# Performance work log

Hardware: AMD Instinct MI355X
Metric: run time of the kernel (lower is better)

## Reference

```python
import jax, jax.numpy as jnp
import numpy as np
import math

D_MODEL = 1024
NUM_HEADS = 16
MAX_LEN = 2048
D_HEAD = D_MODEL // NUM_HEADS
BATCH = 2
SEQ = 2048


def setup_inputs() -> dict:
    root = jax.random.key(0)
    ks = jax.random.split(root, 10)
    s = 1.0 / math.sqrt(D_MODEL)
    return {
        "query": jax.random.normal(ks[0], (BATCH, SEQ, D_MODEL), jnp.float32),
        "key": jax.random.normal(ks[1], (BATCH, SEQ, D_MODEL), jnp.float32),
        "value": jax.random.normal(ks[2], (BATCH, SEQ, D_MODEL), jnp.float32),
        "Wq": jax.random.normal(ks[3], (D_MODEL, D_MODEL), jnp.float32) * s,
        "bq": jax.random.normal(ks[4], (D_MODEL,), jnp.float32) * s,
        "Wk": jax.random.normal(ks[5], (D_MODEL, D_MODEL), jnp.float32) * s,
        "bk": jax.random.normal(ks[6], (D_MODEL,), jnp.float32) * s,
        "Wv": jax.random.normal(ks[7], (D_MODEL, D_MODEL), jnp.float32) * s,
        "bv": jax.random.normal(ks[8], (D_MODEL,), jnp.float32) * s,
        "Er": jax.random.normal(ks[9], (MAX_LEN, D_HEAD), jnp.float32),
    }


def _skew(QEr):
    # QEr: [B, H, S, S] -> pad one zero column on the left, reshape, drop first row
    B, H, R, C = QEr.shape
    padded = jnp.pad(QEr, ((0, 0), (0, 0), (0, 0), (1, 0)))  # [B,H,R,C+1]
    reshaped = padded.reshape(B, H, C + 1, R)
    return reshaped[:, :, 1:, :]  # [B,H,R,C] == Srel


def reference(query, key, value, Wq, bq, Wk, bk, Wv, bv, Er):
    B, S, D = query.shape
    H, dh = NUM_HEADS, D_HEAD
    # nn.Linear: x @ W.T + b
    q = (jnp.einsum("bsd,ed->bse", query, Wq) + bq).reshape(B, S, H, dh).transpose(0, 2, 1, 3)  # [B,H,S,dh]
    k = (jnp.einsum("bsd,ed->bse", key, Wk) + bk).reshape(B, S, H, dh).transpose(0, 2, 1, 3)
    v = (jnp.einsum("bsd,ed->bse", value, Wv) + bv).reshape(B, S, H, dh).transpose(0, 2, 1, 3)
    start = MAX_LEN - S
    Er_s = Er[start:, :]  # [S, dh]
    QEr = jnp.einsum("bhsd,ld->bhsl", q, Er_s)  # [B,H,S,S]
    Srel = _skew(QEr)
    QK = jnp.einsum("bhsd,bhtd->bhst", q, k)
    attn = (QK + Srel) / math.sqrt(dh)
    causal = jnp.tril(jnp.ones((S, S), dtype=bool))
    attn = jnp.where(causal[None, None], attn, -jnp.inf)
    attn = jax.nn.softmax(attn, axis=-1)
    out = jnp.einsum("bhst,bhtd->bhsd", attn, v)  # [B,H,S,dh]
    out = out.transpose(0, 2, 1, 3).reshape(B, S, D)
    return out  # dropout is identity in eval mode
```

## Files before the change

kernel.cpp:

```cpp
#include <hip/hip_runtime.h>
#include <hip/hip_bf16.h>

typedef __attribute__((ext_vector_type(8))) short bf16x8;
typedef __attribute__((ext_vector_type(4))) float f32x4;

#define DEVI __device__ __forceinline__
#define AS1 __attribute__((address_space(1)))
#define AS3 __attribute__((address_space(3)))

constexpr int SEQ_   = 2048;
constexpr int HEADS  = 16;
constexpr int DHEAD  = 64;
constexpr int DMODEL = 1024;

DEVI unsigned short f2bf(float x) {
  __hip_bfloat16 h = __float2bfloat16(x);
  return __builtin_bit_cast(unsigned short, h);
}

DEVI f32x4 MFMA(bf16x8 a, bf16x8 b, f32x4 c) {
  return __builtin_amdgcn_mfma_f32_16x16x32_bf16(a, b, c, 0, 0, 0);
}

DEVI unsigned int cvtpk(float lo, float hi) {
  unsigned int u;
  asm("v_cvt_pk_bf16_f32 %0, %1, %2" : "=v"(u) : "v"(lo), "v"(hi));
  return u;
}

__global__ void conv3_kernel(const float* s0, const float* s1, const float* s2,
                             unsigned short* d0, unsigned short* d1, unsigned short* d2,
                             int n) {
  const float* s = (blockIdx.y == 0) ? s0 : (blockIdx.y == 1) ? s1 : s2;
  unsigned short* d = (blockIdx.y == 0) ? d0 : (blockIdx.y == 1) ? d1 : d2;
  int i = (blockIdx.x * 256 + threadIdx.x) * 8;
  if (i >= n) return;
  const float4* p = (const float4*)(s + i);
  float4 v0 = p[0], v1 = p[1];
  union { unsigned short u[8]; bf16x8 v; } t;
  t.u[0] = f2bf(v0.x); t.u[1] = f2bf(v0.y); t.u[2] = f2bf(v0.z); t.u[3] = f2bf(v0.w);
  t.u[4] = f2bf(v1.x); t.u[5] = f2bf(v1.y); t.u[6] = f2bf(v1.z); t.u[7] = f2bf(v1.w);
  *(bf16x8*)(d + i) = t.v;
}

__global__ void conv4_kernel(const float* s0, const float* s1, const float* s2,
                             const float* s3,
                             unsigned short* d0, unsigned short* d1,
                             unsigned short* d2, unsigned short* d3,
                             int n_w, int n_e) {
  const int y = blockIdx.y;
  const float* s = (y == 0) ? s0 : (y == 1) ? s1 : (y == 2) ? s2 : s3;
  unsigned short* d = (y == 0) ? d0 : (y == 1) ? d1 : (y == 2) ? d2 : d3;
  const int n = (y == 3) ? n_e : n_w;
  int i = (blockIdx.x * 256 + threadIdx.x) * 8;
  if (i >= n) return;
  const float4* p = (const float4*)(s + i);
  float4 v0 = p[0], v1 = p[1];
  union { unsigned short u[8]; bf16x8 v; } t;
  t.u[0] = f2bf(v0.x); t.u[1] = f2bf(v0.y); t.u[2] = f2bf(v0.z); t.u[3] = f2bf(v0.w);
  t.u[4] = f2bf(v1.x); t.u[5] = f2bf(v1.y); t.u[6] = f2bf(v1.z); t.u[7] = f2bf(v1.w);
  *(bf16x8*)(d + i) = t.v;
}

__global__ __launch_bounds__(256) void proj3_kernel(
    const unsigned short* __restrict__ X0, const unsigned short* __restrict__ X1,
    const unsigned short* __restrict__ X2,
    const unsigned short* __restrict__ W0, const unsigned short* __restrict__ W1,
    const unsigned short* __restrict__ W2,
    const float* __restrict__ bi0, const float* __restrict__ bi1,
    const float* __restrict__ bi2,
    unsigned short* __restrict__ o0, unsigned short* __restrict__ o1,
    unsigned short* __restrict__ o2) {
  const int z = blockIdx.z;
  const unsigned short* X = (z == 0) ? X0 : (z == 1) ? X1 : X2;
  const unsigned short* W = (z == 0) ? W0 : (z == 1) ? W1 : W2;
  const float* bias        = (z == 0) ? bi0 : (z == 1) ? bi1 : bi2;
  unsigned short* out      = (z == 0) ? o0 : (z == 1) ? o1 : o2;

  __shared__ unsigned short Abuf[2][128 * 32];
  __shared__ unsigned short Bbuf[2][128 * 32];
  const int tid  = threadIdx.x;
  const int lane = tid & 63, wv = tid >> 6;
  const int q = lane >> 4, r = lane & 15;
  const int wrow = wv >> 1, wcol = wv & 1;
  const int rowA0 = blockIdx.x * 128, colB0 = blockIdx.y * 128;

  const char* Ag = (const char*)(X + (size_t)rowA0 * DMODEL);
  const char* Bg = (const char*)(W + (size_t)colB0 * DMODEL);

  f32x4 acc[4][4] = {};

  auto stage = [&](int ks, int buf) {
    const int koff = ks * 64;
#pragma unroll
    for (int i = 0; i < 2; ++i) {
      const int b   = (i * 256 + tid) * 16;
      const int row = b >> 6, col = b & 63;
      __builtin_amdgcn_global_load_lds(
          (const AS1 void*)(Ag + (size_t)row * (DMODEL * 2) + koff + col),
          (AS3 void*)((char*)&Abuf[buf][0] + i * 4096 + wv * 1024),
          16, 0, 0);
      __builtin_amdgcn_global_load_lds(
          (const AS1 void*)(Bg + (size_t)row * (DMODEL * 2) + koff + col),
          (AS3 void*)((char*)&Bbuf[buf][0] + i * 4096 + wv * 1024),
          16, 0, 0);
    }
  };

  stage(0, 0);
  for (int ks = 0; ks < 32; ++ks) {
    __syncthreads();
    if (ks + 1 < 32) stage(ks + 1, (ks + 1) & 1);
    const unsigned short* A  = &Abuf[ks & 1][0];
    const unsigned short* Bt = &Bbuf[ks & 1][0];
    bf16x8 af[4], bfr[4];
#pragma unroll
    for (int t = 0; t < 4; ++t) {
      af[t]  = *(const bf16x8*)(A  + (wrow * 64 + t * 16 + r) * 32 + q * 8);
      bfr[t] = *(const bf16x8*)(Bt + (wcol * 64 + t * 16 + r) * 32 + q * 8);
    }
#pragma unroll
    for (int m = 0; m < 4; ++m)
#pragma unroll
      for (int n = 0; n < 4; ++n)
        acc[m][n] = MFMA(af[m], bfr[n], acc[m][n]);
  }

#pragma unroll
  for (int m = 0; m < 4; ++m) {
#pragma unroll
    for (int n = 0; n < 4; ++n) {
      const int e  = colB0 + wcol * 64 + n * 16 + r;
      const float bv = bias[e];
      const int h = e >> 6, dd = e & 63;
      const int nrow0 = rowA0 + wrow * 64 + m * 16 + q * 4;
      const int bb = nrow0 >> 11, ss0 = nrow0 & 2047;
      const size_t bh = (size_t)(bb * HEADS + h);
      if (z == 0) {
#pragma unroll
        for (int j = 0; j < 4; ++j)
          out[(bh * SEQ_ + (ss0 + j)) * DHEAD + dd] = f2bf((acc[m][n][j] + bv) * 0.125f);
      } else if (z == 1) {
#pragma unroll
        for (int j = 0; j < 4; ++j) {
          const int s = ss0 + j;
          const size_t off = (bh * 64 + (size_t)(s >> 5)) * 2048
                           + (size_t)(((dd >> 5) * 2 + ((s >> 4) & 1)) * 512)
                           + (size_t)(((((dd & 31) >> 3) << 4) + (s & 15)) * 8)
                           + (dd & 7);
          out[off] = f2bf(acc[m][n][j] + bv);
        }
      } else {
#pragma unroll
        for (int j = 0; j < 4; ++j) {
          const int s = ss0 + j;
          const int tile64 = s >> 6, t = s & 63;
          const int tp = 4 * (t & 15) + (t >> 4);
          const int tc = tp >> 5, u = tp & 31;
          const int ln = ((u >> 3) << 4) | (dd & 15);
          const size_t off = (bh * 32 + (size_t)tile64) * 4096
                           + (size_t)(tc * 2048 + (dd >> 4) * 512 + ln * 8 + (u & 7));
          out[off] = f2bf(acc[m][n][j] + bv);
        }
      }
    }
  }
}

struct ErSet { bf16x8 e[8]; };

__global__ __launch_bounds__(256, 2) void attn_kernel(
    const unsigned short* __restrict__ qb, const unsigned short* __restrict__ kt,
    const unsigned short* __restrict__ vt, const unsigned short* __restrict__ Er,
    float* __restrict__ out, float* __restrict__ pO1, float* __restrict__ pL) {
  __shared__ unsigned short k_lds[3][4096];
  __shared__ unsigned short v_lds[3][4096];
  __shared__ unsigned short p_lds[4][32][68];

  const int tid  = threadIdx.x;
  const int lane = tid & 63, wv = tid >> 6;
  const int q = lane >> 4, r = lane & 15;

  const int lid = blockIdx.x;
  const int xcd = lid & 7, idx = lid >> 3;
  const int bh  = (xcd << 2) | (idx & 3);
  const int jb  = idx >> 2;
  const int p = jb >> 1, role = jb & 1;
  const int bb = bh >> 4, hh = bh & 15;

  const unsigned short* qbh = qb + (size_t)bh * SEQ_ * DHEAD;
  const char* ktb = (const char*)(kt + (size_t)bh * 64 * 2048);
  const char* vtb = (const char*)(vt + (size_t)bh * 32 * 4096);
  const f32x4 zero4 = {0.f, 0.f, 0.f, 0.f};

  const char* sgbase = (wv < 2) ? ktb : vtb;
  char* sdst0 = (char*)((wv < 2) ? &k_lds[0][0] : &v_lds[0][0]);
  const int shalf = (wv & 1) * 4096;
  const int soff  = lane * 16;

  auto stageKV = [&](int it, int buf) {
    const char* src = sgbase + (size_t)it * 8192 + shalf + soff;
    char* dst = sdst0 + buf * 8192 + shalf;
#pragma unroll
    for (int c = 0; c < 4; ++c)
      __builtin_amdgcn_global_load_lds((const AS1 void*)(src + c * 1024),
                                       (AS3 void*)(dst + c * 1024), 16, 0, 0);
  };

  auto run_strip = [&](int T, int it0, int it1, float* po, float* pl) {
    const int s0 = T * 128 + wv * 32;
    __syncthreads();
    stageKV(it0, 0);

    bf16x8 qf[2][2];
#pragma unroll
    for (int rt = 0; rt < 2; ++rt) {
      qf[rt][0] = *(const bf16x8*)(qbh + (size_t)(s0 + rt * 16 + r) * DHEAD + q * 8);
      qf[rt][1] = *(const bf16x8*)(qbh + (size_t)(s0 + rt * 16 + r) * DHEAD + 32 + q * 8);
    }

    f32x4 qer[2][6];
    {
      const int lb0 = 2016 + it0 * 64 - s0;
#pragma unroll
      for (int m = 0; m < 2; ++m) {
        int l = lb0 + m * 16 + r; l = l < 2047 ? l : 2047;
        bf16x8 e0 = *(const bf16x8*)(Er + (size_t)l * DHEAD + q * 8);
        bf16x8 e1 = *(const bf16x8*)(Er + (size_t)l * DHEAD + 32 + q * 8);
#pragma unroll
        for (int rt = 0; rt < 2; ++rt)
          qer[rt][m] = MFMA(qf[rt][1], e1, MFMA(qf[rt][0], e0, zero4));
      }
    }

    auto loadE = [&](ErSet& es, int it) {
      const int lb = 2016 + it * 64 - s0;
#pragma unroll
      for (int mi = 0; mi < 4; ++mi) {
        int l = lb + 32 + mi * 16 + r;
        l = l < 2047 ? l : 2047;
        es.e[mi * 2 + 0] = *(const bf16x8*)(Er + (size_t)l * DHEAD + q * 8);
        es.e[mi * 2 + 1] = *(const bf16x8*)(Er + (size_t)l * DHEAD + 32 + q * 8);
      }
    };

    f32x4 oacc[2][4] = {};
    float lpart[2][4] = {};

    auto body = [&](int it, int cur, const ErSet& es) {
      const int t0 = it * 64;
      if (t0 > s0 + 31) return;
      const unsigned short* KL = &k_lds[cur][0];
      const unsigned short* VL = &v_lds[cur][0];

      bf16x8 kf[4][2];
#pragma unroll
      for (int ct = 0; ct < 4; ++ct)
#pragma unroll
        for (int kc = 0; kc < 2; ++kc)
          kf[ct][kc] = *(const bf16x8*)(KL + (ct >> 1) * 2048 + (kc * 2 + (ct & 1)) * 512 + lane * 8);

      f32x4 s4[2][4];
      __builtin_amdgcn_s_setprio(1);
#pragma unroll
      for (int rt = 0; rt < 2; ++rt)
#pragma unroll
        for (int ct = 0; ct < 4; ++ct)
          s4[rt][ct] = MFMA(qf[rt][1], kf[ct][1], MFMA(qf[rt][0], kf[ct][0], zero4));
#pragma unroll
      for (int rt = 0; rt < 2; ++rt)
#pragma unroll
        for (int mi = 0; mi < 4; ++mi)
          qer[rt][2 + mi] = MFMA(qf[rt][1], es.e[mi * 2 + 1],
                                 MFMA(qf[rt][0], es.e[mi * 2 + 0], zero4));
      __builtin_amdgcn_s_setprio(0);

      const int d0 = t0 - s0;
#pragma unroll
      for (int rt = 0; rt < 2; ++rt) {
        const int a = 1 - rt;
#pragma unroll
        for (int j = 0; j < 4; ++j) {
          unsigned int pkA = cvtpk(qer[rt][a][j],     qer[rt][a + 1][j]);
          unsigned int pkB = cvtpk(qer[rt][a + 2][j], qer[rt][a + 3][j]);
          const float  s5f = qer[rt][a + 4][j];
          const int srcl = (q << 4) | ((15 + r - q * 4 - j) & 15);
          unsigned int A = (unsigned int)__shfl((int)pkA, srcl);
          unsigned int B = (unsigned int)__shfl((int)pkB, srcl);
          const float g4 = __shfl(s5f, srcl);
          const float g0 = __builtin_bit_cast(float, A << 16);
          const float g1 = __builtin_bit_cast(float, A & 0xffff0000u);
          const float g2 = __builtin_bit_cast(float, B << 16);
          const float g3 = __builtin_bit_cast(float, B & 0xffff0000u);
          const bool hi = (r > q * 4 + j);
          const float b0 = hi ? g1 : g0;
          const float b1 = hi ? g2 : g1;
          const float b2 = hi ? g3 : g2;
          const float b3 = hi ? g4 : g3;
          const int A_ = rt * 16 + q * 4 + j - r - d0;
          const float p0 = (A_ >= 0)  ? __expf(s4[rt][0][j] + b0) : 0.f;
          const float p1 = (A_ >= 16) ? __expf(s4[rt][1][j] + b1) : 0.f;
          const float p2 = (A_ >= 32) ? __expf(s4[rt][2][j] + b2) : 0.f;
          const float p3 = (A_ >= 48) ? __expf(s4[rt][3][j] + b3) : 0.f;
          lpart[rt][j] += (p0 + p1) + (p2 + p3);
          const int sl = rt * 16 + q * 4 + j;
          const unsigned long long pw =
              (unsigned long long)cvtpk(p0, p1) |
              ((unsigned long long)cvtpk(p2, p3) << 32);
          *(unsigned long long*)&p_lds[wv][sl][4 * r] = pw;
        }
      }

      bf16x8 vf[4][2];
#pragma unroll
      for (int dc = 0; dc < 4; ++dc)
#pragma unroll
        for (int tc = 0; tc < 2; ++tc)
          vf[dc][tc] = *(const bf16x8*)(VL + tc * 2048 + dc * 512 + lane * 8);
      __builtin_amdgcn_s_setprio(1);
#pragma unroll
      for (int rt = 0; rt < 2; ++rt) {
        bf16x8 pf0 = *(const bf16x8*)(&p_lds[wv][rt * 16 + r][0] + q * 8);
        bf16x8 pf1 = *(const bf16x8*)(&p_lds[wv][rt * 16 + r][0] + 32 + q * 8);
#pragma unroll
        for (int dc = 0; dc < 4; ++dc)
          oacc[rt][dc] = MFMA(pf1, vf[dc][1], MFMA(pf0, vf[dc][0], oacc[rt][dc]));
      }
      __builtin_amdgcn_s_setprio(0);

#pragma unroll
      for (int rt = 0; rt < 2; ++rt) { qer[rt][0] = qer[rt][4]; qer[rt][1] = qer[rt][5]; }
    };

    ErSet eA, eB;
    loadE(eA, it0);

    int it = it0, cur = 0;
    while (true) {
      int nx = cur + 1; if (nx == 3) nx = 0;
      int itn = (it + 1 < it1) ? it + 1 : it1 - 1;
      stageKV(itn, nx);
      loadE(eB, itn);
      asm volatile("s_waitcnt vmcnt(12)\n\ts_barrier" ::: "memory");
      body(it, cur, eA);
      cur = nx;
      if (++it >= it1) break;
      nx = cur + 1; if (nx == 3) nx = 0;
      itn = (it + 1 < it1) ? it + 1 : it1 - 1;
      stageKV(itn, nx);
      loadE(eA, itn);
      asm volatile("s_waitcnt vmcnt(12)\n\ts_barrier" ::: "memory");
      body(it, cur, eB);
      cur = nx;
      if (++it >= it1) break;
    }

#pragma unroll
    for (int rt = 0; rt < 2; ++rt)
#pragma unroll
      for (int j = 0; j < 4; ++j) {
        float ls = lpart[rt][j];
#pragma unroll
        for (int d = 1; d < 16; d <<= 1) ls += __shfl_xor(ls, d);
        const int row = wv * 32 + rt * 16 + q * 4 + j;
        if (po) {
#pragma unroll
          for (int dc = 0; dc < 4; ++dc)
            po[(size_t)row * 64 + dc * 16 + r] = oacc[rt][dc][j];
        } else {
          const int ss = T * 128 + row;
#pragma unroll
          for (int dc = 0; dc < 4; ++dc)
            out[((size_t)(bb * SEQ_ + ss)) * DMODEL + hh * DHEAD + dc * 16 + r] = oacc[rt][dc][j];
        }
        if (r == 0) pl[row] = ls;
      }
  };

  int TA, a1, TB, b0, b1;
  if (role == 0) { TA = 15 - p; a1 = 16 - p; TB = p;      b0 = p + 1;  b1 = 2 * p + 2; }
  else           { TA = p;      a1 = p + 1;  TB = 15 - p; b0 = 16 - p; b1 = 32 - 2 * p; }

  run_strip(TA, 0, a1, nullptr,
            pL + ((size_t)(bh * 16 + TA)) * 256);
  run_strip(TB, b0, b1, pO1 + ((size_t)(bh * 16 + TB)) * 8192,
            pL + ((size_t)(bh * 16 + TB)) * 256 + 128);
}

__global__ __launch_bounds__(256) void reduce_kernel(const float* __restrict__ pO1,
                                                     const float* __restrict__ pL,
                                                     float* __restrict__ out) {
  const int slot = blockIdx.x;
  const int bh = slot >> 4, T = slot & 15;
  const int bb = bh >> 4, hh = bh & 15;
  const int tid = threadIdx.x;
  const int row = tid >> 1, half = (tid & 1) * 32;

  const float l0 = pL[(size_t)slot * 256 + row];
  const float l1 = pL[(size_t)slot * 256 + 128 + row];
  const float inv = 1.0f / (l0 + l1);

  float* a = out + ((size_t)(bb * SEQ_) + T * 128 + row) * DMODEL + hh * DHEAD + half;
  const float* b = pO1 + (size_t)slot * 8192 + row * 64 + half;
#pragma unroll
  for (int k = 0; k < 8; ++k) {
    float4 x = ((const float4*)a)[k];
    float4 y = ((const float4*)b)[k];
    float4 o;
    o.x = (x.x + y.x) * inv; o.y = (x.y + y.y) * inv;
    o.z = (x.z + y.z) * inv; o.w = (x.w + y.w) * inv;
    ((float4*)a)[k] = o;
  }
}

extern "C" void kernel_launch(void* const* d_in, const int* in_sizes, int n_in,
                              void* d_out, int out_size, void* d_ws, size_t ws_size,
                              hipStream_t stream) {
  const float* query = (const float*)d_in[0];
  const float* key   = (const float*)d_in[1];
  const float* value = (const float*)d_in[2];
  const float* Wq    = (const float*)d_in[3];
  const float* bq    = (const float*)d_in[4];
  const float* Wk    = (const float*)d_in[5];
  const float* bk    = (const float*)d_in[6];
  const float* Wv    = (const float*)d_in[7];
  const float* bv    = (const float*)d_in[8];
  const float* Er    = (const float*)d_in[9];

  char* ws = (char*)d_ws;
  unsigned short* qb   = (unsigned short*)(ws + (0u  << 20));
  unsigned short* ktil = (unsigned short*)(ws + (8u  << 20));
  unsigned short* vtil = (unsigned short*)(ws + (16u << 20));
  float*          pO1  = (float*)(ws + (24u << 20));
  float*          pL   = (float*)(ws + (40u << 20));
  unsigned short* Xq   = (unsigned short*)(ws + (32u << 20));
  unsigned short* Xk   = (unsigned short*)(ws + (40u << 20));
  unsigned short* Xv   = (unsigned short*)(ws + (48u << 20));
  unsigned short* Wqb  = (unsigned short*)(ws + (56u << 20));
  unsigned short* Wkb  = (unsigned short*)(ws + (58u << 20));
  unsigned short* Wvb  = (unsigned short*)(ws + (60u << 20));
  unsigned short* Erb  = (unsigned short*)(ws + (62u << 20));

  conv3_kernel<<<dim3(2048, 3), 256, 0, stream>>>(query, key, value, Xq, Xk, Xv,
                                                  2 * SEQ_ * DMODEL);
  conv4_kernel<<<dim3(512, 4), 256, 0, stream>>>(Wq, Wk, Wv, Er,
                                                 Wqb, Wkb, Wvb, Erb,
                                                 DMODEL * DMODEL, SEQ_ * DHEAD);

  proj3_kernel<<<dim3(32, 8, 3), 256, 0, stream>>>(Xq, Xk, Xv, Wqb, Wkb, Wvb,
                                                   bq, bk, bv, qb, ktil, vtil);

  attn_kernel<<<dim3(512), 256, 0, stream>>>(qb, ktil, vtil, Erb,
                                             (float*)d_out, pO1, pL);

  reduce_kernel<<<dim3(512), 256, 0, stream>>>(pO1, pL, (float*)d_out);
}
```

Measured before the change: 141.3 us.

## Split causal attention strips into four KV chunks with 32-wide tiles and bf16 partials

Every query strip now splits its causal KV range into four equal chunks, each handled by a separate block. The grid doubles to 1024 blocks, and the reduce kernel merges four partial outputs. Tiles shrink from 64 to 32 keys, the V layout from the projection changes to match, and LDS buffers are halved so the launch bound can allow four blocks per CU. Partial outputs are stored as bf16, and exp is replaced by exp2 with log2(e) folded into the Q scale. This is meant to balance causal work across blocks and raise occupancy, at the cost of more partial-output traffic, smaller MFMA batches per step, and bf16 rounding of the partials.

```diff
diff --git a/kernel.cpp b/kernel.cpp
--- a/kernel.cpp
+++ b/kernel.cpp
@@ -139,7 +139,8 @@
       if (z == 0) {
 #pragma unroll
         for (int j = 0; j < 4; ++j)
-          out[(bh * SEQ_ + (ss0 + j)) * DHEAD + dd] = f2bf((acc[m][n][j] + bv) * 0.125f);
+          out[(bh * SEQ_ + (ss0 + j)) * DHEAD + dd] =
+              f2bf((acc[m][n][j] + bv) * 0.1803368801111244f);
       } else if (z == 1) {
 #pragma unroll
         for (int j = 0; j < 4; ++j) {
@@ -154,12 +155,12 @@
 #pragma unroll
         for (int j = 0; j < 4; ++j) {
           const int s = ss0 + j;
-          const int tile64 = s >> 6, t = s & 63;
-          const int tp = 4 * (t & 15) + (t >> 4);
-          const int tc = tp >> 5, u = tp & 31;
-          const int ln = ((u >> 3) << 4) | (dd & 15);
-          const size_t off = (bh * 32 + (size_t)tile64) * 4096
-                           + (size_t)(tc * 2048 + (dd >> 4) * 512 + ln * 8 + (u & 7));
+          const int t = s & 31;
+          const int tp = 2 * (t & 15) + (t >> 4);
+          const size_t off = (bh * 64 + (size_t)(s >> 5)) * 2048
+                           + (size_t)((dd >> 4) * 512)
+                           + (size_t)(((((tp >> 3) << 4) | (dd & 15))) * 8)
+                           + (tp & 7);
           out[off] = f2bf(acc[m][n][j] + bv);
         }
       }
@@ -167,15 +168,15 @@
   }
 }
 
-struct ErSet { bf16x8 e[8]; };
-
-__global__ __launch_bounds__(256, 2) void attn_kernel(
+struct ErSet { bf16x8 e[4]; };
+
+__global__ __launch_bounds__(256, 4) void attn_kernel(
     const unsigned short* __restrict__ qb, const unsigned short* __restrict__ kt,
     const unsigned short* __restrict__ vt, const unsigned short* __restrict__ Er,
-    float* __restrict__ out, float* __restrict__ pO1, float* __restrict__ pL) {
-  __shared__ unsigned short k_lds[3][4096];
-  __shared__ unsigned short v_lds[3][4096];
-  __shared__ unsigned short p_lds[4][32][68];
+    unsigned short* __restrict__ pO, float* __restrict__ pL) {
+  __shared__ unsigned short k_lds[3][2048];
+  __shared__ unsigned short v_lds[3][2048];
+  __shared__ unsigned short p_lds[4][32][40];
 
   const int tid  = threadIdx.x;
   const int lane = tid & 63, wv = tid >> 6;
@@ -184,33 +185,32 @@
   const int lid = blockIdx.x;
   const int xcd = lid & 7, idx = lid >> 3;
   const int bh  = (xcd << 2) | (idx & 3);
-  const int jb  = idx >> 2;
-  const int p = jb >> 1, role = jb & 1;
-  const int bb = bh >> 4, hh = bh & 15;
+  const int rest = idx >> 2;
+  const int p = rest >> 2, qq = rest & 3;
 
   const unsigned short* qbh = qb + (size_t)bh * SEQ_ * DHEAD;
   const char* ktb = (const char*)(kt + (size_t)bh * 64 * 2048);
-  const char* vtb = (const char*)(vt + (size_t)bh * 32 * 4096);
+  const char* vtb = (const char*)(vt + (size_t)bh * 64 * 2048);
   const f32x4 zero4 = {0.f, 0.f, 0.f, 0.f};
 
   const char* sgbase = (wv < 2) ? ktb : vtb;
   char* sdst0 = (char*)((wv < 2) ? &k_lds[0][0] : &v_lds[0][0]);
-  const int shalf = (wv & 1) * 4096;
+  const int shalf = (wv & 1) * 2048;
   const int soff  = lane * 16;
 
-  auto stageKV = [&](int it, int buf) {
-    const char* src = sgbase + (size_t)it * 8192 + shalf + soff;
-    char* dst = sdst0 + buf * 8192 + shalf;
-#pragma unroll
-    for (int c = 0; c < 4; ++c)
-      __builtin_amdgcn_global_load_lds((const AS1 void*)(src + c * 1024),
-                                       (AS3 void*)(dst + c * 1024), 16, 0, 0);
+  auto stage = [&](int it, int buf) {
+    const char* src = sgbase + (size_t)it * 4096 + shalf + soff;
+    char* dst = sdst0 + buf * 4096 + shalf;
+    __builtin_amdgcn_global_load_lds((const AS1 void*)(src),
+                                     (AS3 void*)(dst), 16, 0, 0);
+    __builtin_amdgcn_global_load_lds((const AS1 void*)(src + 1024),
+                                     (AS3 void*)(dst + 1024), 16, 0, 0);
   };
 
-  auto run_strip = [&](int T, int it0, int it1, float* po, float* pl) {
+  auto run_strip = [&](int T, int it0, int it1, unsigned short* po, float* pl) {
     const int s0 = T * 128 + wv * 32;
     __syncthreads();
-    stageKV(it0, 0);
+    stage(it0, 0);
 
     bf16x8 qf[2][2];
 #pragma unroll
@@ -219,12 +219,12 @@
       qf[rt][1] = *(const bf16x8*)(qbh + (size_t)(s0 + rt * 16 + r) * DHEAD + 32 + q * 8);
     }
 
-    f32x4 qer[2][6];
+    f32x4 qer[2][4];
     {
-      const int lb0 = 2016 + it0 * 64 - s0;
+      const int B0 = 2016 + 32 * it0 - s0;
 #pragma unroll
       for (int m = 0; m < 2; ++m) {
-        int l = lb0 + m * 16 + r; l = l < 2047 ? l : 2047;
+        int l = B0 + m * 16 + r; l = l < 2047 ? l : 2047;
         bf16x8 e0 = *(const bf16x8*)(Er + (size_t)l * DHEAD + q * 8);
         bf16x8 e1 = *(const bf16x8*)(Er + (size_t)l * DHEAD + 32 + q * 8);
 #pragma unroll
@@ -234,10 +234,10 @@
     }
 
     auto loadE = [&](ErSet& es, int it) {
-      const int lb = 2016 + it * 64 - s0;
-#pragma unroll
-      for (int mi = 0; mi < 4; ++mi) {
-        int l = lb + 32 + mi * 16 + r;
+      const int B0 = 2016 + 32 * it - s0;
+#pragma unroll
+      for (int mi = 0; mi < 2; ++mi) {
+        int l = B0 + 32 + mi * 16 + r;
         l = l < 2047 ? l : 2047;
         es.e[mi * 2 + 0] = *(const bf16x8*)(Er + (size_t)l * DHEAD + q * 8);
         es.e[mi * 2 + 1] = *(const bf16x8*)(Er + (size_t)l * DHEAD + 32 + q * 8);
@@ -248,29 +248,29 @@
     float lpart[2][4] = {};
 
     auto body = [&](int it, int cur, const ErSet& es) {
-      const int t0 = it * 64;
+      const int t0 = it * 32;
       if (t0 > s0 + 31) return;
       const unsigned short* KL = &k_lds[cur][0];
       const unsigned short* VL = &v_lds[cur][0];
 
-      bf16x8 kf[4][2];
-#pragma unroll
-      for (int ct = 0; ct < 4; ++ct)
+      bf16x8 kf[2][2];
+#pragma unroll
+      for (int ct = 0; ct < 2; ++ct)
 #pragma unroll
         for (int kc = 0; kc < 2; ++kc)
-          kf[ct][kc] = *(const bf16x8*)(KL + (ct >> 1) * 2048 + (kc * 2 + (ct & 1)) * 512 + lane * 8);
-
-      f32x4 s4[2][4];
+          kf[ct][kc] = *(const bf16x8*)(KL + (kc * 2 + ct) * 512 + lane * 8);
+
+      f32x4 s4[2][2];
       __builtin_amdgcn_s_setprio(1);
 #pragma unroll
       for (int rt = 0; rt < 2; ++rt)
 #pragma unroll
-        for (int ct = 0; ct < 4; ++ct)
+        for (int ct = 0; ct < 2; ++ct)
           s4[rt][ct] = MFMA(qf[rt][1], kf[ct][1], MFMA(qf[rt][0], kf[ct][0], zero4));
 #pragma unroll
       for (int rt = 0; rt < 2; ++rt)
 #pragma unroll
-        for (int mi = 0; mi < 4; ++mi)
+        for (int mi = 0; mi < 2; ++mi)
           qer[rt][2 + mi] = MFMA(qf[rt][1], es.e[mi * 2 + 1],
                                  MFMA(qf[rt][0], es.e[mi * 2 + 0], zero4));
       __builtin_amdgcn_s_setprio(0);
@@ -281,55 +281,41 @@
         const int a = 1 - rt;
 #pragma unroll
         for (int j = 0; j < 4; ++j) {
-          unsigned int pkA = cvtpk(qer[rt][a][j],     qer[rt][a + 1][j]);
-          unsigned int pkB = cvtpk(qer[rt][a + 2][j], qer[rt][a + 3][j]);
-          const float  s5f = qer[rt][a + 4][j];
+          const unsigned int pk = cvtpk(qer[rt][a][j], qer[rt][a + 1][j]);
+          const float f2 = qer[rt][a + 2][j];
           const int srcl = (q << 4) | ((15 + r - q * 4 - j) & 15);
-          unsigned int A = (unsigned int)__shfl((int)pkA, srcl);
-          unsigned int B = (unsigned int)__shfl((int)pkB, srcl);
-          const float g4 = __shfl(s5f, srcl);
+          const unsigned int A = (unsigned int)__shfl((int)pk, srcl);
+          const float g2 = __shfl(f2, srcl);
           const float g0 = __builtin_bit_cast(float, A << 16);
           const float g1 = __builtin_bit_cast(float, A & 0xffff0000u);
-          const float g2 = __builtin_bit_cast(float, B << 16);
-          const float g3 = __builtin_bit_cast(float, B & 0xffff0000u);
           const bool hi = (r > q * 4 + j);
           const float b0 = hi ? g1 : g0;
           const float b1 = hi ? g2 : g1;
-          const float b2 = hi ? g3 : g2;
-          const float b3 = hi ? g4 : g3;
           const int A_ = rt * 16 + q * 4 + j - r - d0;
-          const float p0 = (A_ >= 0)  ? __expf(s4[rt][0][j] + b0) : 0.f;
-          const float p1 = (A_ >= 16) ? __expf(s4[rt][1][j] + b1) : 0.f;
-          const float p2 = (A_ >= 32) ? __expf(s4[rt][2][j] + b2) : 0.f;
-          const float p3 = (A_ >= 48) ? __expf(s4[rt][3][j] + b3) : 0.f;
-          lpart[rt][j] += (p0 + p1) + (p2 + p3);
+          const float p0 = (A_ >= 0)  ? exp2f(s4[rt][0][j] + b0) : 0.f;
+          const float p1 = (A_ >= 16) ? exp2f(s4[rt][1][j] + b1) : 0.f;
+          lpart[rt][j] += p0 + p1;
           const int sl = rt * 16 + q * 4 + j;
-          const unsigned long long pw =
-              (unsigned long long)cvtpk(p0, p1) |
-              ((unsigned long long)cvtpk(p2, p3) << 32);
-          *(unsigned long long*)&p_lds[wv][sl][4 * r] = pw;
+          *(unsigned int*)&p_lds[wv][sl][2 * r] = cvtpk(p0, p1);
         }
       }
 
-      bf16x8 vf[4][2];
+      bf16x8 vf[4];
 #pragma unroll
       for (int dc = 0; dc < 4; ++dc)
-#pragma unroll
-        for (int tc = 0; tc < 2; ++tc)
-          vf[dc][tc] = *(const bf16x8*)(VL + tc * 2048 + dc * 512 + lane * 8);
+        vf[dc] = *(const bf16x8*)(VL + dc * 512 + lane * 8);
       __builtin_amdgcn_s_setprio(1);
 #pragma unroll
       for (int rt = 0; rt < 2; ++rt) {
-        bf16x8 pf0 = *(const bf16x8*)(&p_lds[wv][rt * 16 + r][0] + q * 8);
-        bf16x8 pf1 = *(const bf16x8*)(&p_lds[wv][rt * 16 + r][0] + 32 + q * 8);
+        bf16x8 pf = *(const bf16x8*)(&p_lds[wv][rt * 16 + r][0] + q * 8);
 #pragma unroll
         for (int dc = 0; dc < 4; ++dc)
-          oacc[rt][dc] = MFMA(pf1, vf[dc][1], MFMA(pf0, vf[dc][0], oacc[rt][dc]));
+          oacc[rt][dc] = MFMA(pf, vf[dc], oacc[rt][dc]);
       }
       __builtin_amdgcn_s_setprio(0);
 
 #pragma unroll
-      for (int rt = 0; rt < 2; ++rt) { qer[rt][0] = qer[rt][4]; qer[rt][1] = qer[rt][5]; }
+      for (int rt = 0; rt < 2; ++rt) { qer[rt][0] = qer[rt][2]; qer[rt][1] = qer[rt][3]; }
     };
 
     ErSet eA, eB;
@@ -339,17 +325,17 @@
     while (true) {
       int nx = cur + 1; if (nx == 3) nx = 0;
       int itn = (it + 1 < it1) ? it + 1 : it1 - 1;
-      stageKV(itn, nx);
+      stage(itn, nx);
       loadE(eB, itn);
-      asm volatile("s_waitcnt vmcnt(12)\n\ts_barrier" ::: "memory");
+      asm volatile("s_waitcnt vmcnt(6)\n\ts_barrier" ::: "memory");
       body(it, cur, eA);
       cur = nx;
       if (++it >= it1) break;
       nx = cur + 1; if (nx == 3) nx = 0;
       itn = (it + 1 < it1) ? it + 1 : it1 - 1;
-      stageKV(itn, nx);
+      stage(itn, nx);
       loadE(eA, itn);
-      asm volatile("s_waitcnt vmcnt(12)\n\ts_barrier" ::: "memory");
+      asm volatile("s_waitcnt vmcnt(6)\n\ts_barrier" ::: "memory");
       body(it, cur, eB);
       cur = nx;
       if (++it >= it1) break;
@@ -363,31 +349,23 @@
 #pragma unroll
         for (int d = 1; d < 16; d <<= 1) ls += __shfl_xor(ls, d);
         const int row = wv * 32 + rt * 16 + q * 4 + j;
-        if (po) {
-#pragma unroll
-          for (int dc = 0; dc < 4; ++dc)
-            po[(size_t)row * 64 + dc * 16 + r] = oacc[rt][dc][j];
-        } else {
-          const int ss = T * 128 + row;
-#pragma unroll
-          for (int dc = 0; dc < 4; ++dc)
-            out[((size_t)(bb * SEQ_ + ss)) * DMODEL + hh * DHEAD + dc * 16 + r] = oacc[rt][dc][j];
-        }
+#pragma unroll
+        for (int dc = 0; dc < 4; ++dc)
+          po[(size_t)row * 64 + dc * 16 + r] = f2bf(oacc[rt][dc][j]);
         if (r == 0) pl[row] = ls;
       }
   };
 
-  int TA, a1, TB, b0, b1;
-  if (role == 0) { TA = 15 - p; a1 = 16 - p; TB = p;      b0 = p + 1;  b1 = 2 * p + 2; }
-  else           { TA = p;      a1 = p + 1;  TB = 15 - p; b0 = 16 - p; b1 = 32 - 2 * p; }
-
-  run_strip(TA, 0, a1, nullptr,
-            pL + ((size_t)(bh * 16 + TA)) * 256);
-  run_strip(TB, b0, b1, pO1 + ((size_t)(bh * 16 + TB)) * 8192,
-            pL + ((size_t)(bh * 16 + TB)) * 256 + 128);
-}
-
-__global__ __launch_bounds__(256) void reduce_kernel(const float* __restrict__ pO1,
+  const int TA = 15 - p, lenA = 16 - p;
+  const int TB = p,      lenB = p + 1;
+  const size_t slotA = ((size_t)bh * 16 + TA) * 4 + qq;
+  const size_t slotB = ((size_t)bh * 16 + TB) * 4 + qq;
+
+  run_strip(TA, qq * lenA, (qq + 1) * lenA, pO + slotA * 8192, pL + slotA * 128);
+  run_strip(TB, qq * lenB, (qq + 1) * lenB, pO + slotB * 8192, pL + slotB * 128);
+}
+
+__global__ __launch_bounds__(256) void reduce_kernel(const unsigned short* __restrict__ pO,
                                                      const float* __restrict__ pL,
                                                      float* __restrict__ out) {
   const int slot = blockIdx.x;
@@ -396,20 +374,32 @@
   const int tid = threadIdx.x;
   const int row = tid >> 1, half = (tid & 1) * 32;
 
-  const float l0 = pL[(size_t)slot * 256 + row];
-  const float l1 = pL[(size_t)slot * 256 + 128 + row];
-  const float inv = 1.0f / (l0 + l1);
-
-  float* a = out + ((size_t)(bb * SEQ_) + T * 128 + row) * DMODEL + hh * DHEAD + half;
-  const float* b = pO1 + (size_t)slot * 8192 + row * 64 + half;
-#pragma unroll
-  for (int k = 0; k < 8; ++k) {
-    float4 x = ((const float4*)a)[k];
-    float4 y = ((const float4*)b)[k];
+  float l = 0.f;
+#pragma unroll
+  for (int k = 0; k < 4; ++k) l += pL[((size_t)slot * 4 + k) * 128 + row];
+  const float inv = 1.0f / l;
+
+  float acc[32] = {};
+#pragma unroll
+  for (int k = 0; k < 4; ++k) {
+    const unsigned short* src = pO + ((size_t)slot * 4 + k) * 8192 + row * 64 + half;
+#pragma unroll
+    for (int c = 0; c < 4; ++c) {
+      union { bf16x8 v; unsigned short u[8]; } w;
+      w.v = *(const bf16x8*)(src + c * 8);
+#pragma unroll
+      for (int e = 0; e < 8; ++e)
+        acc[c * 8 + e] += __builtin_bit_cast(float, (unsigned int)w.u[e] << 16);
+    }
+  }
+
+  float* dst = out + ((size_t)(bb * SEQ_) + T * 128 + row) * DMODEL + hh * DHEAD + half;
+#pragma unroll
+  for (int c = 0; c < 8; ++c) {
     float4 o;
-    o.x = (x.x + y.x) * inv; o.y = (x.y + y.y) * inv;
-    o.z = (x.z + y.z) * inv; o.w = (x.w + y.w) * inv;
-    ((float4*)a)[k] = o;
+    o.x = acc[c * 4 + 0] * inv; o.y = acc[c * 4 + 1] * inv;
+    o.z = acc[c * 4 + 2] * inv; o.w = acc[c * 4 + 3] * inv;
+    ((float4*)dst)[c] = o;
   }
 }
 
@@ -431,8 +421,8 @@
   unsigned short* qb   = (unsigned short*)(ws + (0u  << 20));
   unsigned short* ktil = (unsigned short*)(ws + (8u  << 20));
   unsigned short* vtil = (unsigned short*)(ws + (16u << 20));
-  float*          pO1  = (float*)(ws + (24u << 20));
-  float*          pL   = (float*)(ws + (40u << 20));
+  unsigned short* pO   = (unsigned short*)(ws + (24u << 20));
+  float*          pL   = (float*)(ws + (56u << 20));
   unsigned short* Xq   = (unsigned short*)(ws + (32u << 20));
   unsigned short* Xk   = (unsigned short*)(ws + (40u << 20));
   unsigned short* Xv   = (unsigned short*)(ws + (48u << 20));
@@ -450,8 +440,7 @@
   proj3_kernel<<<dim3(32, 8, 3), 256, 0, stream>>>(Xq, Xk, Xv, Wqb, Wkb, Wvb,
                                                    bq, bk, bv, qb, ktil, vtil);
 
-  attn_kernel<<<dim3(512), 256, 0, stream>>>(qb, ktil, vtil, Erb,
-                                             (float*)d_out, pO1, pL);
-
-  reduce_kernel<<<dim3(512), 256, 0, stream>>>(pO1, pL, (float*)d_out);
-}
+  attn_kernel<<<dim3(1024), 256, 0, stream>>>(qb, ktil, vtil, Erb, pO, pL);
+
+  reduce_kernel<<<dim3(512), 256, 0, stream>>>(pO, pL, (float*)d_out);
+}
```

Result: slower. 243.7 us (+72.5%).
